# Performance work log

Hardware: AMD Instinct MI355X
Metric: run time of the kernel (lower is better)

## Reference

```python
import jax, jax.numpy as jnp
import numpy as np
from jax import lax

K = 8            # number of object slots
H = 250          # hidden / fc_size
EPS = 1e-5
DN = ('NCHW', 'OIHW', 'NCHW')


def ln_all(x):
    # F.layer_norm over all non-batch dims, no affine params (torch init: w=1,b=0)
    ax = tuple(range(1, x.ndim))
    m = jnp.mean(x, ax, keepdims=True)
    v = jnp.var(x, ax, keepdims=True)
    return (x - m) * lax.rsqrt(v + EPS)


def ln_last(x):
    # nn.LayerNorm(feat) -> last dim only
    m = jnp.mean(x, -1, keepdims=True)
    v = jnp.var(x, -1, keepdims=True)
    return (x - m) * lax.rsqrt(v + EPS)


def conv(x, w, b):
    # torch Conv2d(k=4, s=2, p=1), NCHW
    y = lax.conv_general_dilated(x, w, (2, 2), [(1, 1), (1, 1)], dimension_numbers=DN)
    return y + b[None, :, None, None]


def up4(x):
    return jnp.repeat(jnp.repeat(x, 4, axis=2), 4, axis=3)


def setup_inputs():
    ks = jax.random.split(jax.random.key(0), 20)
    bk = 48 * K
    p = lambda i, shape, s: jax.random.normal(ks[i], shape, jnp.float32) * s
    z = lambda n: jnp.zeros((n,), jnp.float32)
    return dict(
        x=p(0, (bk, 4096), 1.0),
        state=p(1, (bk, H), 1.0),
        # encoder convs (OIHW) + fc
        c1w=p(2, (16, 1, 4, 4), 0.25), c1b=z(16),
        c2w=p(3, (32, 16, 4, 4), 0.06), c2b=z(32),
        c3w=p(4, (64, 32, 4, 4), 0.04), c3b=z(64),
        efc_w=p(5, (4096, 512), 0.016), efc_b=z(512),
        # R_NEM (weights stored as [in, out])
        renc_w=p(6, (H, H), 0.06), renc_b=z(H),
        core_w=p(7, (2 * H, H), 0.045), core_b=z(H),
        ctx_w=p(8, (H, H), 0.06), ctx_b=z(H),
        att1_w=p(9, (H, 100), 0.06), att1_b=z(100),
        att2_w=p(10, (100, 1), 0.1), att2_b=z(1),
        out_w=p(11, (2 * H + 512, H), 0.03), out_b=z(H),
        # decoder fcs + convs
        dfc1_w=p(12, (H, 512), 0.06), dfc1_b=z(512),
        dfc2_w=p(13, (512, 4096), 0.045), dfc2_b=z(4096),
        d1w=p(14, (32, 64, 4, 4), 0.03), d1b=z(32),
        d2w=p(15, (16, 32, 4, 4), 0.045), d2b=z(16),
        d3w=p(16, (1, 16, 4, 4), 0.06), d3b=z(1),
    )


def reference(x, state, c1w, c1b, c2w, c2b, c3w, c3b, efc_w, efc_b,
              renc_w, renc_b, core_w, core_b, ctx_w, ctx_b,
              att1_w, att1_b, att2_w, att2_b, out_w, out_b,
              dfc1_w, dfc1_b, dfc2_w, dfc2_b, d1w, d1b, d2w, d2b, d3w, d3b):
    bk = x.shape[0]
    b = bk // K

    # ---------------- EncoderLayer ----------------
    def inwrap(h, w, bias):  # InputWrapper conv branch: NHWC -> permute(0,3,2,1) -> conv -> back
        y = conv(jnp.transpose(h, (0, 3, 2, 1)), w, bias)
        return jax.nn.elu(ln_all(jnp.transpose(y, (0, 3, 2, 1))))

    h = x.reshape(bk, 64, 64, 1)
    h = inwrap(h, c1w, c1b)                 # (bk,32,32,16)
    h = inwrap(h, c2w, c2b)                 # (bk,16,16,32)
    h = inwrap(h, c3w, c3b)                 # (bk,8,8,64)
    h = h.reshape(bk, -1)                   # (bk,4096)
    h = jax.nn.elu(ln_last(h @ efc_w + efc_b))   # (bk,512)

    # ---------------- R_NEM (RecurrentLayer) ----------------
    s1 = jax.nn.relu(ln_last(state @ renc_w + renc_b))   # (bk,H)
    s1r = s1.reshape(b, K, H)
    idx = np.array([[j for j in range(K) if j != i] for i in range(K)])  # (K,K-1)
    cs = s1r[:, idx, :]                                    # context: (b,K,K-1,H)
    fs = jnp.broadcast_to(s1r[:, :, None, :], cs.shape)    # focus copies
    pair = jnp.concatenate([fs, cs], axis=-1)              # (b,K,K-1,2H)
    core = jax.nn.relu(ln_last(pair @ core_w + core_b))    # (b,K,K-1,H)
    ctx = jax.nn.relu(ln_last(core @ ctx_w + ctx_b))       # (b,K,K-1,H)
    att = jax.nn.sigmoid(jnp.tanh(ln_last(core @ att1_w + att1_b)) @ att2_w + att2_b)  # (b,K,K-1,1)
    effect = jnp.sum(ctx * att, axis=2).reshape(bk, H)     # attention-weighted sum over K-1
    total = jnp.concatenate([s1, effect, h], axis=1)       # (bk, 2H+512)
    new_state = total @ out_w + out_b                      # (bk,H)
    xr = jax.nn.sigmoid(ln_last(new_state))
    state_out = jax.nn.sigmoid(new_state)

    # ---------------- DecoderLayer ----------------
    d = jax.nn.relu(ln_last(xr @ dfc1_w + dfc1_b))         # (bk,512)
    d = jax.nn.relu(ln_last(d @ dfc2_w + dfc2_b))          # (bk,4096)
    d = d.reshape(bk, 8, 8, 64)

    def outwrap(t, w, bias):
        y = conv(up4(jnp.transpose(t, (0, 3, 2, 1))), w, bias)
        return jnp.transpose(y, (0, 3, 2, 1))

    d = jax.nn.relu(ln_all(outwrap(d, d1w, d1b)))          # (bk,16,16,32)
    d = jax.nn.relu(ln_all(outwrap(d, d2w, d2b)))          # (bk,32,32,16)
    d = jax.nn.sigmoid(outwrap(d, d3w, d3b))               # (bk,64,64,1), no LN
    x_out = d.reshape(bk, -1)                              # (bk,4096)
    return x_out, state_out
```

## Files before the change

### kernel.cpp

```cpp
#include <hip/hip_runtime.h>
#include <hip/hip_bf16.h>
#include <math.h>

typedef __attribute__((ext_vector_type(8))) short bf16x8;
typedef __attribute__((ext_vector_type(4))) float f32x4;

__device__ __forceinline__ float eluf(float v){ return v > 0.f ? v : expm1f(v); }
__device__ __forceinline__ float sigf(float v){ return 1.f/(1.f+expf(-v)); }
__device__ __forceinline__ unsigned short f2bf(float f){
  unsigned u = __float_as_uint(f);
  u += 0x7FFFu + ((u >> 16) & 1u);
  return (unsigned short)(u >> 16);
}
__device__ __forceinline__ float bf2f(short s){
  return __uint_as_float(((unsigned)(unsigned short)s) << 16);
}

__device__ __forceinline__ void block_reduce2(float& a, float& b, float* sbuf){
  __syncthreads();
  for (int off = 32; off; off >>= 1){
    a += __shfl_down(a, off);
    b += __shfl_down(b, off);
  }
  int lane = threadIdx.x & 63, w = threadIdx.x >> 6;
  if (lane == 0){ sbuf[2*w] = a; sbuf[2*w+1] = b; }
  __syncthreads();
  if (threadIdx.x == 0){
    int nw = blockDim.x >> 6;
    float sa = 0.f, sb = 0.f;
    for (int i = 0; i < nw; i++){ sa += sbuf[2*i]; sb += sbuf[2*i+1]; }
    sbuf[0] = sa; sbuf[1] = sb;
  }
  __syncthreads();
  a = sbuf[0]; b = sbuf[1];
}

__device__ __forceinline__ float fold_sum(const float* __restrict__ w, int O, int I,
                                          int o, int i, int pa, int pb, int da, int db){
  float s = 0.f;
  for (int kh = 0; kh < 4; kh++){
    bool inh = (pb==0) ? (db==0 ? (kh==0) : (kh>=1)) : (db==0 ? (kh<=2) : (kh==3));
    if (!inh) continue;
    for (int kw = 0; kw < 4; kw++){
      bool inw = (pa==0) ? (da==0 ? (kw==0) : (kw>=1)) : (da==0 ? (kw<=2) : (kw==3));
      if (!inw) continue;
      s += w[((o*I + i)*4 + kh)*4 + kw];
    }
  }
  return s;
}
__device__ __forceinline__ void fold_elem(const float* __restrict__ w, float* __restrict__ CW,
                                          int O, int I, int l){
  int o = l % O; int q = l / O;
  int da = q & 1, db = (q>>1)&1, pa = (q>>2)&1, pb = (q>>3)&1, i = q>>4;
  CW[(((pb*2+pa)*4 + db*2+da)*I + i)*O + o] = fold_sum(w, O, I, o, i, pa, pb, da, db);
}
__device__ __forceinline__ void cvtc2_elem(const float* __restrict__ w, short* __restrict__ D, int l){
  int i = l & 15, t = (l>>4) & 15, o = l>>8;
  D[l] = (short)f2bf(w[(o*16 + i)*16 + t]);
}
__device__ __forceinline__ void cvtc3_elem(const float* __restrict__ w, short* __restrict__ D, int l){
  int i = l & 31, t = (l>>5) & 15, o = l>>9;
  D[l] = (short)f2bf(w[(o*32 + i)*16 + t]);
}
__device__ __forceinline__ void foldd1_elem(const float* __restrict__ w, short* __restrict__ D, int l){
  int i = l & 63, tap = (l>>6)&3, o = (l>>8)&31, ph = l>>13;
  D[l] = (short)f2bf(fold_sum(w, 32, 64, o, i, ph&1, ph>>1, tap&1, tap>>1));
}
__device__ __forceinline__ void foldd2_elem(const float* __restrict__ w, short* __restrict__ D, int l){
  int i = l & 31, tap = (l>>5)&3, o = (l>>7)&15, ph = l>>11;
  D[l] = (short)f2bf(fold_sum(w, 16, 32, o, i, ph&1, ph>>1, tap&1, tap>>1));
}

__global__ __launch_bounds__(256) void prep_combined(
  const float* __restrict__ efc,  short* __restrict__ Defc,
  const float* __restrict__ dfc2, short* __restrict__ Ddfc2,
  const float* __restrict__ outw, short* __restrict__ Dout,
  const float* __restrict__ corew,short* __restrict__ Dcore,
  const float* __restrict__ dfc1, short* __restrict__ Ddfc1,
  const float* __restrict__ renc, short* __restrict__ Drenc,
  const float* __restrict__ ctx,  short* __restrict__ Dctx,
  const float* __restrict__ att1, short* __restrict__ Datt1,
  const float* __restrict__ d3w, float* __restrict__ CWT3,
  const float* __restrict__ c2w, short* __restrict__ BtC2,
  const float* __restrict__ c3w, short* __restrict__ BtC3,
  const float* __restrict__ d1w, short* __restrict__ BD1,
  const float* __restrict__ d2w, short* __restrict__ BD2,
  const float* __restrict__ state, short* __restrict__ SBF,
  short* __restrict__ TOTb)
{
  int bx = blockIdx.x;
  if (bx >= 1192){
    const int F3=256, P2=F3+8192, P3=P2+32768, P4=P3+32768, P5=P4+8192,
              ST=P5+98304, TOTAL=ST+4608;
    for (int l = (bx-1192)*256 + threadIdx.x; l < TOTAL; l += 256*256){
      if (l < F3)      fold_elem(d3w, CWT3, 1, 16, l);
      else if (l < P2) cvtc2_elem(c2w, BtC2, l - F3);
      else if (l < P3) cvtc3_elem(c3w, BtC3, l - P2);
      else if (l < P4) foldd1_elem(d1w, BD1, l - P3);
      else if (l < P5) foldd2_elem(d2w, BD2, l - P4);
      else if (l < ST){
        int q = l - P5;
        int n = q >> 8, k = q & 255;
        SBF[q] = (k < 250) ? (short)f2bf(state[n*250 + k]) : (short)0;
      } else {
        int q = l - ST;
        int row = q / 12, cc = q % 12;
        int col = cc < 6 ? 250 + cc : 506 + (cc - 6);
        TOTb[row*1024 + col] = 0;
      }
    }
    return;
  }
  const float* W; short* D; int K, N, Kp, base, mode = 0;
  if      (bx < 512) { W=efc;  D=Defc;  K=4096; N=512;  Kp=4096; base=0;    }
  else if (bx < 1024){ W=dfc2; D=Ddfc2; K=512;  N=4096; Kp=512;  base=512;  }
  else if (bx < 1088){ W=outw; D=Dout;  K=1012; N=250;  Kp=1024; base=1024; mode=2; }
  else if (bx < 1120){ W=corew;D=Dcore; K=500;  N=250;  Kp=512;  base=1088; mode=1; }
  else if (bx < 1152){ W=dfc1; D=Ddfc1; K=250;  N=512;  Kp=256;  base=1120; }
  else if (bx < 1168){ W=renc; D=Drenc; K=250;  N=250;  Kp=256;  base=1152; }
  else if (bx < 1184){ W=ctx;  D=Dctx;  K=250;  N=250;  Kp=256;  base=1168; }
  else               { W=att1; D=Datt1; K=250;  N=100;  Kp=256;  base=1184; }
  int t = bx - base;
  int tpr = Kp >> 6;
  int tk = t % tpr, tn = t / tpr;
  __shared__ short tile[64][65];
  int c = threadIdx.x & 63, r4 = threadIdx.x >> 6;
  int n0 = tn*64, k0 = tk*64;
  #pragma unroll 4
  for (int p = 0; p < 16; p++){
    int r = r4*16 + p;
    int k = k0 + r, n = n0 + c;
    int ksrc = k; bool valid;
    if (mode == 0) valid = (k < K);
    else if (mode == 1){ valid = (k < 250) || (k >= 256 && k < 506); ksrc = k < 256 ? k : k - 6; }
    else { valid = (k < 250) || (k >= 256 && k < 506) || (k >= 512);
           ksrc = k < 256 ? k : (k < 512 ? k - 6 : k - 12); }
    float v = (valid && n < N) ? W[(size_t)ksrc*N + n] : 0.f;
    tile[c][r] = (short)f2bf(v);
  }
  __syncthreads();
  #pragma unroll 4
  for (int p = 0; p < 16; p++){
    int nn = r4*16 + p;
    int n = n0 + nn;
    if (n < N) D[(size_t)n*Kp + k0 + c] = tile[nn][c];
  }
}

__global__ __launch_bounds__(256) void gemm_mfma(
    const short* __restrict__ Ab, const short* __restrict__ Bt,
    float* __restrict__ P, int M, int N, int Kp, int Kc)
{
  __shared__ __align__(16) short As[64*32];
  __shared__ __align__(16) short Bs[64*32];
  int tid = threadIdx.x;
  int bm = blockIdx.y*64, bn = blockIdx.x*64;
  int kb = blockIdx.z * Kc;
  int kend = kb + Kc;

  int r = tid >> 2, c = tid & 3;
  const short* Arow = Ab + (size_t)(bm + r)*Kp;
  int gn = bn + r;
  bool bval = gn < N;
  const short* Brow = Bt + (size_t)gn*Kp;

  uint4 hA, hB;
  auto load_regs = [&](int k0){
    hA = *(const uint4*)&Arow[k0 + c*8];
    hB = bval ? *(const uint4*)&Brow[k0 + c*8] : make_uint4(0,0,0,0);
  };
  auto write_lds = [&](){
    *(uint4*)&As[r*32 + c*8] = hA;
    *(uint4*)&Bs[r*32 + c*8] = hB;
  };

  int wave = tid >> 6;
  int ln = tid & 15, quad = (tid >> 4) & 3;
  int wr = (wave >> 1) * 32, wc = (wave & 1) * 32;

  f32x4 zero = {0.f, 0.f, 0.f, 0.f};
  f32x4 acc[2][2] = {{zero, zero}, {zero, zero}};

  load_regs(kb);
  write_lds();
  __syncthreads();
  for (int k0 = kb; k0 < kend; k0 += 32){
    int nxt = k0 + 32;
    if (nxt < kend) load_regs(nxt);
    bf16x8 a0 = *(const bf16x8*)&As[(wr +      ln)*32 + quad*8];
    bf16x8 a1 = *(const bf16x8*)&As[(wr + 16 + ln)*32 + quad*8];
    bf16x8 b0 = *(const bf16x8*)&Bs[(wc +      ln)*32 + quad*8];
    bf16x8 b1 = *(const bf16x8*)&Bs[(wc + 16 + ln)*32 + quad*8];
    acc[0][0] = __builtin_amdgcn_mfma_f32_16x16x32_bf16(a0, b0, acc[0][0], 0, 0, 0);
    acc[0][1] = __builtin_amdgcn_mfma_f32_16x16x32_bf16(a0, b1, acc[0][1], 0, 0, 0);
    acc[1][0] = __builtin_amdgcn_mfma_f32_16x16x32_bf16(a1, b0, acc[1][0], 0, 0, 0);
    acc[1][1] = __builtin_amdgcn_mfma_f32_16x16x32_bf16(a1, b1, acc[1][1], 0, 0, 0);
    __syncthreads();
    if (nxt < kend){ write_lds(); __syncthreads(); }
  }

  float* Pout = P + (size_t)blockIdx.z*M*N;
  #pragma unroll
  for (int t = 0; t < 2; t++)
    #pragma unroll
    for (int u = 0; u < 2; u++)
      #pragma unroll
      for (int j = 0; j < 4; j++){
        int row = bm + wr + t*16 + quad*4 + j;
        int col = bn + wc + u*16 + ln;
        if (col < N) Pout[(size_t)row*N + col] = acc[t][u][j];
      }
}

__global__ __launch_bounds__(256) void gemm_core_mfma(
    const short* __restrict__ Tb, const short* __restrict__ Bt,
    float* __restrict__ P, int M, int N, int Kc)
{
  __shared__ __align__(16) short As[64*32];
  __shared__ __align__(16) short Bs[64*32];
  int tid = threadIdx.x;
  int bm = blockIdx.y*64, bn = blockIdx.x*64;
  int kb = blockIdx.z * Kc;
  int kend = kb + Kc;

  int r = tid >> 2, c = tid & 3;
  int gr = bm + r;
  int jj2 = gr % 7, fi2 = gr / 7;
  int ii = fi2 & 7, j2 = fi2 >> 3;
  int jidx = jj2 < ii ? jj2 : jj2 + 1;
  const short* own = Tb + (size_t)fi2*1024;
  const short* oth = Tb + (size_t)(j2*8 + jidx)*1024;
  int gn = bn + r;
  bool bval = gn < N;
  const short* Brow = Bt + (size_t)gn*512;

  uint4 hA, hB;
  auto load_regs = [&](int k0){
    int kk = k0 + c*8;
    const short* src = (kk & 256) ? oth : own;
    hA = *(const uint4*)&src[kk & 255];
    hB = bval ? *(const uint4*)&Brow[kk] : make_uint4(0,0,0,0);
  };
  auto write_lds = [&](){
    *(uint4*)&As[r*32 + c*8] = hA;
    *(uint4*)&Bs[r*32 + c*8] = hB;
  };

  int wave = tid >> 6;
  int ln = tid & 15, quad = (tid >> 4) & 3;
  int wr = (wave >> 1) * 32, wc = (wave & 1) * 32;

  f32x4 zero = {0.f, 0.f, 0.f, 0.f};
  f32x4 acc[2][2] = {{zero, zero}, {zero, zero}};

  load_regs(kb);
  write_lds();
  __syncthreads();
  for (int k0 = kb; k0 < kend; k0 += 32){
    int nxt = k0 + 32;
    if (nxt < kend) load_regs(nxt);
    bf16x8 a0 = *(const bf16x8*)&As[(wr +      ln)*32 + quad*8];
    bf16x8 a1 = *(const bf16x8*)&As[(wr + 16 + ln)*32 + quad*8];
    bf16x8 b0 = *(const bf16x8*)&Bs[(wc +      ln)*32 + quad*8];
    bf16x8 b1 = *(const bf16x8*)&Bs[(wc + 16 + ln)*32 + quad*8];
    acc[0][0] = __builtin_amdgcn_mfma_f32_16x16x32_bf16(a0, b0, acc[0][0], 0, 0, 0);
    acc[0][1] = __builtin_amdgcn_mfma_f32_16x16x32_bf16(a0, b1, acc[0][1], 0, 0, 0);
    acc[1][0] = __builtin_amdgcn_mfma_f32_16x16x32_bf16(a1, b0, acc[1][0], 0, 0, 0);
    acc[1][1] = __builtin_amdgcn_mfma_f32_16x16x32_bf16(a1, b1, acc[1][1], 0, 0, 0);
    __syncthreads();
    if (nxt < kend){ write_lds(); __syncthreads(); }
  }

  float* Pout = P + (size_t)blockIdx.z*M*N;
  #pragma unroll
  for (int t = 0; t < 2; t++)
    #pragma unroll
    for (int u = 0; u < 2; u++)
      #pragma unroll
      for (int j = 0; j < 4; j++){
        int row = bm + wr + t*16 + quad*4 + j;
        int col = bn + wc + u*16 + ln;
        if (col < N) Pout[(size_t)row*N + col] = acc[t][u][j];
      }
}

__global__ __launch_bounds__(256) void reduce_ln(
    const float* __restrict__ Pp, const float* __restrict__ bias,
    void* __restrict__ outp, int M, int N, int KS, int os, int act, int obf)
{
  __shared__ float rowbuf[4096];
  __shared__ float sbuf[16];
  int row = blockIdx.x;
  size_t MN = (size_t)M*N;
  float s = 0.f, s2 = 0.f;
  for (int c = threadIdx.x; c < N; c += 256){
    float v = bias[c];
    for (int ks = 0; ks < KS; ks++) v += Pp[ks*MN + (size_t)row*N + c];
    rowbuf[c] = v; s += v; s2 += v*v;
  }
  block_reduce2(s, s2, sbuf);
  float m = s / N;
  float r = rsqrtf(s2/N - m*m + 1e-5f);
  for (int c = threadIdx.x; c < N; c += 256){
    float v = (rowbuf[c]-m)*r;
    if (act == 1) v = fmaxf(v, 0.f);
    else if (act == 2) v = eluf(v);
    else if (act == 3) v = tanhf(v);
    if (obf) ((short*)outp)[(size_t)row*os + c] = f2bf(v);
    else     ((float*)outp)[(size_t)row*os + c] = v;
  }
}

__global__ __launch_bounds__(256) void reduce_ns(
    const float* __restrict__ Pp, const float* __restrict__ bias,
    short* __restrict__ XRb, float* __restrict__ so, int M, int N, int KS)
{
  __shared__ float rowbuf[256];
  __shared__ float sbuf[16];
  int row = blockIdx.x;
  size_t MN = (size_t)M*N;
  float s = 0.f, s2 = 0.f;
  for (int c = threadIdx.x; c < N; c += 256){
    float v = bias[c];
    for (int ks = 0; ks < KS; ks++) v += Pp[ks*MN + (size_t)row*N + c];
    rowbuf[c] = v; s += v; s2 += v*v;
  }
  block_reduce2(s, s2, sbuf);
  float m = s / N;
  float r = rsqrtf(s2/N - m*m + 1e-5f);
  for (int c = threadIdx.x; c < N; c += 256){
    float v = rowbuf[c];
    XRb[(size_t)row*256 + c] = f2bf(sigf((v-m)*r));
    so[(size_t)row*N + c] = sigf(v);
  }
}

__global__ __launch_bounds__(448) void ctx_att_effect(
    const float* __restrict__ Pc, const float* __restrict__ ctx_b,
    const float* __restrict__ Pa, const float* __restrict__ att1_b,
    const float* __restrict__ w2, const float* __restrict__ b2,
    short* __restrict__ tot)
{
  __shared__ float ctxs[7][250];
  __shared__ float att_s[7];
  int fi = blockIdx.x, tid = threadIdx.x;
  int jj = tid >> 6, lane = tid & 63;
  const size_t MN = (size_t)2688*250, MN2 = (size_t)2688*100;
  int row = fi*7 + jj;
  float vv[4];
  float s = 0.f, s2 = 0.f;
  #pragma unroll
  for (int t = 0; t < 4; t++){
    int c = lane + t*64;
    float v = 0.f;
    if (c < 250) v = ctx_b[c] + Pc[(size_t)row*250 + c] + Pc[MN + (size_t)row*250 + c];
    vv[t] = v; s += v; s2 += v*v;
  }
  #pragma unroll
  for (int off = 32; off; off >>= 1){ s += __shfl_down(s, off); s2 += __shfl_down(s2, off); }
  s = __shfl(s, 0); s2 = __shfl(s2, 0);
  float m = s*(1.f/250.f);
  float r = rsqrtf(s2*(1.f/250.f) - m*m + 1e-5f);
  #pragma unroll
  for (int t = 0; t < 4; t++){
    int c = lane + t*64;
    if (c < 250) ctxs[jj][c] = fmaxf((vv[t]-m)*r, 0.f);
  }
  float va[2];
  s = 0.f; s2 = 0.f;
  #pragma unroll
  for (int t = 0; t < 2; t++){
    int c = lane + t*64;
    float v = 0.f;
    if (c < 100){
      v = att1_b[c];
      #pragma unroll
      for (int ks = 0; ks < 4; ks++) v += Pa[ks*MN2 + (size_t)row*100 + c];
    }
    va[t] = v; s += v; s2 += v*v;
  }
  #pragma unroll
  for (int off = 32; off; off >>= 1){ s += __shfl_down(s, off); s2 += __shfl_down(s2, off); }
  s = __shfl(s, 0); s2 = __shfl(s2, 0);
  m = s*0.01f;
  r = rsqrtf(s2*0.01f - m*m + 1e-5f);
  float d = 0.f;
  #pragma unroll
  for (int t = 0; t < 2; t++){
    int c = lane + t*64;
    if (c < 100) d += tanhf((va[t]-m)*r)*w2[c];
  }
  #pragma unroll
  for (int off = 32; off; off >>= 1) d += __shfl_down(d, off);
  if (lane == 0) att_s[jj] = sigf(d + b2[0]);
  __syncthreads();
  for (int h = tid; h < 250; h += 448){
    float sum = 0.f;
    #pragma unroll
    for (int q = 0; q < 7; q++) sum += ctxs[q][h]*att_s[q];
    tot[(size_t)fi*1024 + 256 + h] = f2bf(sum);
  }
}

__global__ __launch_bounds__(256) void enc_conv1_ig(
    const float* __restrict__ x, const float* __restrict__ w, const float* __restrict__ bias,
    short* __restrict__ outp)
{
  __shared__ __align__(16) float in_t[66*68];
  __shared__ short rawb[16384];
  __shared__ float sbuf[16];
  int n = blockIdx.x, tid = threadIdx.x;
  for (int l = tid; l < 66*68; l += 256) in_t[l] = 0.f;
  __syncthreads();
  const float* xin = x + (size_t)n*4096;
  for (int l4 = tid; l4 < 1024; l4 += 256){
    float4 v = *(const float4*)&xin[l4*4];
    int aa = (l4*4) >> 6, bb = (l4*4) & 63;
    float* dst = &in_t[(aa+1)*68 + bb + 1];
    dst[0]=v.x; dst[1]=v.y; dst[2]=v.z; dst[3]=v.w;
  }
  int o = tid & 15;
  float wr[16];
  #pragma unroll
  for (int t = 0; t < 16; t++) wr[t] = w[o*16 + t];
  float bv = bias[o];
  __syncthreads();
  float s = 0.f, s2 = 0.f;
  for (int r = 0; r < 64; r++){
    int idx = tid + (r<<8);
    int bq = (idx>>4)&31, aq = idx>>9;
    int a0 = 2*aq, b0 = 2*bq;
    float acc = bv;
    #pragma unroll
    for (int kw = 0; kw < 4; kw++){
      const float* row = &in_t[(a0+kw)*68 + b0];
      float2 p0 = *(const float2*)&row[0];
      float2 p1 = *(const float2*)&row[2];
      acc += p0.x*wr[0*4+kw] + p0.y*wr[1*4+kw] + p1.x*wr[2*4+kw] + p1.y*wr[3*4+kw];
    }
    rawb[idx] = f2bf(acc);
    s += acc; s2 += acc*acc;
  }
  block_reduce2(s, s2, sbuf);
  float m = s*(1.f/16384.f);
  float rs = rsqrtf(s2*(1.f/16384.f) - m*m + 1e-5f);
  short* op = outp + (size_t)n*16384;
  for (int l = tid; l < 16384; l += 256){
    float v = bf2f(rawb[l]);
    op[l] = f2bf(eluf((v-m)*rs));
  }
}

__global__ __launch_bounds__(256) void enc_conv23_mfma(
    const short* __restrict__ in, const short* __restrict__ Bt2, const float* __restrict__ bias2,
    const short* __restrict__ Bt3, const float* __restrict__ bias3, short* __restrict__ outp)
{
  __shared__ __align__(16) short smem[34*34*16];
  __shared__ float sbuf[16];
  int n = blockIdx.x, tid = threadIdx.x;
  for (int l = tid; l < 34*34*16/4; l += 256) ((unsigned long long*)smem)[l] = 0ull;
  __syncthreads();
  const short* ip = in + (size_t)n*16384;
  for (int l = tid; l < 4096; l += 256){
    int i4 = l & 3, bb = (l>>2) & 31, aa = l>>7;
    *(uint2*)&smem[((aa+1)*34 + (bb+1))*16 + i4*4] = *(const uint2*)&ip[aa*512 + bb*16 + i4*4];
  }
  int wave = tid>>6, ln = tid&15, quad = (tid>>4)&3;
  bf16x8 bfr[2][8];
  #pragma unroll
  for (int nt = 0; nt < 2; nt++){
    const short* Brow = Bt2 + (nt*16 + ln)*256;
    #pragma unroll
    for (int ks = 0; ks < 8; ks++)
      bfr[nt][ks] = *(const bf16x8*)&Brow[ks*32 + quad*8];
  }
  __syncthreads();
  f32x4 z = {0.f,0.f,0.f,0.f};
  f32x4 acc[2][4] = {{z,z,z,z},{z,z,z,z}};
  int tapq = quad>>1, io = (quad&1)*8;
  #pragma unroll
  for (int ks = 0; ks < 8; ks++){
    int t = 2*ks + tapq;
    int kh = t>>2, kw = t&3;
    #pragma unroll
    for (int mt = 0; mt < 4; mt++){
      int p = (wave*4 + mt)*16 + ln;
      int oa = p>>4, ob = p&15;
      bf16x8 a = *(const bf16x8*)&smem[((2*oa+kw)*34 + (2*ob+kh))*16 + io];
      acc[0][mt] = __builtin_amdgcn_mfma_f32_16x16x32_bf16(a, bfr[0][ks], acc[0][mt],0,0,0);
      acc[1][mt] = __builtin_amdgcn_mfma_f32_16x16x32_bf16(a, bfr[1][ks], acc[1][mt],0,0,0);
    }
  }
  float s = 0.f, s2 = 0.f;
  #pragma unroll
  for (int nt = 0; nt < 2; nt++){
    float bz = bias2[nt*16 + ln];
    #pragma unroll
    for (int mt = 0; mt < 4; mt++)
      #pragma unroll
      for (int j = 0; j < 4; j++){
        float v = acc[nt][mt][j] + bz;
        acc[nt][mt][j] = v; s += v; s2 += v*v;
      }
  }
  block_reduce2(s, s2, sbuf);
  float m2 = s*(1.f/8192.f);
  float rs2 = rsqrtf(s2*(1.f/8192.f) - m2*m2 + 1e-5f);
  int o3 = wave*16 + ln;
  bf16x8 bfr3[16];
  {
    const short* Brow = Bt3 + o3*512;
    #pragma unroll
    for (int ks = 0; ks < 16; ks++)
      bfr3[ks] = *(const bf16x8*)&Brow[ks*32 + quad*8];
  }
  for (int l = tid; l < 2592; l += 256) ((unsigned long long*)smem)[l] = 0ull;
  __syncthreads();
  #pragma unroll
  for (int nt = 0; nt < 2; nt++){
    int o = nt*16 + ln;
    #pragma unroll
    for (int mt = 0; mt < 4; mt++)
      #pragma unroll
      for (int j = 0; j < 4; j++){
        int p = (wave*4 + mt)*16 + quad*4 + j;
        int oa = p>>4, ob = p&15;
        smem[((oa+1)*18 + (ob+1))*32 + o] = f2bf(eluf((acc[nt][mt][j]-m2)*rs2));
      }
  }
  __syncthreads();
  f32x4 acc3[4] = {z,z,z,z};
  #pragma unroll
  for (int ks = 0; ks < 16; ks++){
    int kh = ks>>2, kw = ks&3;
    #pragma unroll
    for (int mt = 0; mt < 4; mt++){
      int p = mt*16 + ln;
      int oa = p>>3, ob = p&7;
      bf16x8 a = *(const bf16x8*)&smem[((2*oa+kw)*18 + (2*ob+kh))*32 + quad*8];
      acc3[mt] = __builtin_amdgcn_mfma_f32_16x16x32_bf16(a, bfr3[ks], acc3[mt],0,0,0);
    }
  }
  s = 0.f; s2 = 0.f;
  float bz3 = bias3[o3];
  #pragma unroll
  for (int mt = 0; mt < 4; mt++)
    #pragma unroll
    for (int j = 0; j < 4; j++){
      float v = acc3[mt][j] + bz3;
      acc3[mt][j] = v; s += v; s2 += v*v;
    }
  block_reduce2(s, s2, sbuf);
  float m3 = s*(1.f/4096.f);
  float rs3 = rsqrtf(s2*(1.f/4096.f) - m3*m3 + 1e-5f);
  short* op = outp + (size_t)n*4096;
  #pragma unroll
  for (int mt = 0; mt < 4; mt++)
    #pragma unroll
    for (int j = 0; j < 4; j++){
      int p = mt*16 + quad*4 + j;
      int oa = p>>3, ob = p&7;
      op[oa*512 + ob*64 + o3] = f2bf(eluf((acc3[mt][j]-m3)*rs3));
    }
}

__global__ __launch_bounds__(256) void dec_conv12_mfma(
    const short* __restrict__ in, const short* __restrict__ Bd1, const float* __restrict__ bias1,
    const short* __restrict__ Bd2, const float* __restrict__ bias2, short* __restrict__ outp)
{
  __shared__ __align__(16) short smem[18*18*32];
  __shared__ float sbuf[16];
  int n = blockIdx.x, tid = threadIdx.x;
  for (int l = tid; l < 1600; l += 256) ((unsigned long long*)smem)[l] = 0ull;
  __syncthreads();
  const short* ip = in + (size_t)n*4096;
  for (int l = tid; l < 1024; l += 256){
    int i4 = l & 15, sb = (l>>4)&7, sa = l>>7;
    *(uint2*)&smem[((sa+1)*10 + (sb+1))*64 + i4*4] = *(const uint2*)&ip[sa*512 + sb*64 + i4*4];
  }
  int wave = tid>>6, ln = tid&15, quad = (tid>>4)&3;
  int pa = wave & 1, pb = wave >> 1;
  bf16x8 bfr1[2][8];
  #pragma unroll
  for (int nt = 0; nt < 2; nt++){
    const short* Brow = Bd1 + (wave*32 + nt*16 + ln)*256;
    #pragma unroll
    for (int ks = 0; ks < 8; ks++)
      bfr1[nt][ks] = *(const bf16x8*)&Brow[ks*32 + quad*8];
  }
  __syncthreads();
  f32x4 z = {0.f,0.f,0.f,0.f};
  f32x4 acc[2][4] = {{z,z,z,z},{z,z,z,z}};
  #pragma unroll
  for (int ks = 0; ks < 8; ks++){
    int tap = ks>>1, ibase = (ks&1)*32 + quad*8;
    int da = tap & 1, db = tap >> 1;
    #pragma unroll
    for (int mt = 0; mt < 4; mt++){
      int p = mt*16 + ln;
      int ta = p>>3, tb = p&7;
      bf16x8 a = *(const bf16x8*)&smem[((ta+da+pa)*10 + (tb+db+pb))*64 + ibase];
      acc[0][mt] = __builtin_amdgcn_mfma_f32_16x16x32_bf16(a, bfr1[0][ks], acc[0][mt],0,0,0);
      acc[1][mt] = __builtin_amdgcn_mfma_f32_16x16x32_bf16(a, bfr1[1][ks], acc[1][mt],0,0,0);
    }
  }
  float s = 0.f, s2 = 0.f;
  #pragma unroll
  for (int nt = 0; nt < 2; nt++){
    float bz = bias1[nt*16 + ln];
    #pragma unroll
    for (int mt = 0; mt < 4; mt++)
      #pragma unroll
      for (int j = 0; j < 4; j++){
        float v = acc[nt][mt][j] + bz;
        acc[nt][mt][j] = v; s += v; s2 += v*v;
      }
  }
  block_reduce2(s, s2, sbuf);
  float m1 = s*(1.f/8192.f);
  float rs1 = rsqrtf(s2*(1.f/8192.f) - m1*m1 + 1e-5f);
  bf16x8 bfr2[4];
  {
    const short* Brow = Bd2 + (wave*16 + ln)*128;
    #pragma unroll
    for (int ks = 0; ks < 4; ks++)
      bfr2[ks] = *(const bf16x8*)&Brow[ks*32 + quad*8];
  }
  for (int l = tid; l < 2592; l += 256) ((unsigned long long*)smem)[l] = 0ull;
  __syncthreads();
  #pragma unroll
  for (int nt = 0; nt < 2; nt++){
    int o = nt*16 + ln;
    #pragma unroll
    for (int mt = 0; mt < 4; mt++)
      #pragma unroll
      for (int j = 0; j < 4; j++){
        int p = mt*16 + quad*4 + j;
        int ta = p>>3, tb = p&7;
        int sa = 2*ta + pa, sb = 2*tb + pb;
        smem[((sa+1)*18 + (sb+1))*32 + o] = f2bf(fmaxf((acc[nt][mt][j]-m1)*rs1, 0.f));
      }
  }
  __syncthreads();
  f32x4 acc2[16] = {z,z,z,z,z,z,z,z,z,z,z,z,z,z,z,z};
  #pragma unroll
  for (int ks = 0; ks < 4; ks++){
    int da = ks & 1, db = ks >> 1;
    #pragma unroll
    for (int mt = 0; mt < 16; mt++){
      int p = mt*16 + ln;
      int ta = p>>4, tb = p&15;
      bf16x8 a = *(const bf16x8*)&smem[((ta+da+pa)*18 + (tb+db+pb))*32 + quad*8];
      acc2[mt] = __builtin_amdgcn_mfma_f32_16x16x32_bf16(a, bfr2[ks], acc2[mt],0,0,0);
    }
  }
  s = 0.f; s2 = 0.f;
  float bz2 = bias2[ln];
  #pragma unroll
  for (int mt = 0; mt < 16; mt++)
    #pragma unroll
    for (int j = 0; j < 4; j++){
      float v = acc2[mt][j] + bz2;
      acc2[mt][j] = v; s += v; s2 += v*v;
    }
  block_reduce2(s, s2, sbuf);
  float m = s*(1.f/16384.f);
  float rs = rsqrtf(s2*(1.f/16384.f) - m*m + 1e-5f);
  short* op = outp + (size_t)n*16384;
  #pragma unroll
  for (int mt = 0; mt < 16; mt++)
    #pragma unroll
    for (int j = 0; j < 4; j++){
      int p = mt*16 + quad*4 + j;
      int ta = p>>4, tb = p&15;
      op[(2*ta+pa)*512 + (2*tb+pb)*16 + ln] = f2bf(fmaxf((acc2[mt][j]-m)*rs, 0.f));
    }
}

__global__ __launch_bounds__(256) void dec_conv3_ig(
    const short* __restrict__ in, const float* __restrict__ CWT, const float* __restrict__ bias,
    float* __restrict__ outp)
{
  __shared__ __align__(16) float in_t[9792];
  __shared__ __align__(16) float wl[256];
  int bx = blockIdx.x;
  int n = bx >> 1, b0 = (bx & 1) * 32, tb0 = b0 >> 1;
  int tid = threadIdx.x;
  const short* ip = in + (size_t)n*16384;
  for (int l = tid; l < 9792; l += 256){
    int i = l & 15, sb = (l >> 4) % 18, sap = l / 288;
    int sa = sap - 1, sbg = tb0 - 1 + sb;
    float v = 0.f;
    if ((unsigned)sa < 32u && (unsigned)sbg < 32u)
      v = bf2f(ip[sa*512 + sbg*16 + i]);
    in_t[(sap*18 + sb)*16 + i] = v;
  }
  for (int l = tid; l < 256; l += 256) wl[l] = CWT[l];
  __syncthreads();
  float bv = bias[0];
  int bl = tid & 31, ath = tid >> 5;
  int b = b0 + bl;
  int tb = b >> 1, pb = b & 1;
  float* op = outp + (size_t)n*4096;
  #pragma unroll
  for (int j = 0; j < 8; j++){
    int a = ath*8 + j;
    int ta = a >> 1, pa = a & 1;
    float4 s4 = make_float4(0.f,0.f,0.f,0.f);
    #pragma unroll
    for (int db = 0; db < 2; db++){
      int sb = tb + db + (pb ? 0 : -1);
      int sbl = sb - (tb0 - 1);
      #pragma unroll
      for (int da = 0; da < 2; da++){
        int sa = ta + da + (pa ? 0 : -1);
        int sap = sa + 1;
        const float4* A4 = (const float4*)&in_t[(sap*18 + sbl)*16];
        const float4* B4 = (const float4*)&wl[((pb*2+pa)*4 + db*2+da)*16];
        #pragma unroll
        for (int q = 0; q < 4; q++){
          float4 av = A4[q], bw = B4[q];
          s4.x += av.x*bw.x; s4.y += av.y*bw.y;
          s4.z += av.z*bw.z; s4.w += av.w*bw.w;
        }
      }
    }
    op[a*64 + b] = sigf(bv + s4.x + s4.y + s4.z + s4.w);
  }
}

extern "C" void kernel_launch(void* const* d_in, const int* in_sizes, int n_in,
                              void* d_out, int out_size, void* d_ws, size_t ws_size,
                              hipStream_t stream) {
  const float* x      = (const float*)d_in[0];
  const float* state  = (const float*)d_in[1];
  const float* c1w    = (const float*)d_in[2];
  const float* c1b    = (const float*)d_in[3];
  const float* c2w    = (const float*)d_in[4];
  const float* c2b    = (const float*)d_in[5];
  const float* c3w    = (const float*)d_in[6];
  const float* c3b    = (const float*)d_in[7];
  const float* efc_w  = (const float*)d_in[8];
  const float* efc_b  = (const float*)d_in[9];
  const float* renc_w = (const float*)d_in[10];
  const float* renc_b = (const float*)d_in[11];
  const float* core_w = (const float*)d_in[12];
  const float* core_b = (const float*)d_in[13];
  const float* ctx_w  = (const float*)d_in[14];
  const float* ctx_b  = (const float*)d_in[15];
  const float* att1_w = (const float*)d_in[16];
  const float* att1_b = (const float*)d_in[17];
  const float* att2_w = (const float*)d_in[18];
  const float* att2_b = (const float*)d_in[19];
  const float* out_w  = (const float*)d_in[20];
  const float* out_b  = (const float*)d_in[21];
  const float* dfc1_w = (const float*)d_in[22];
  const float* dfc1_b = (const float*)d_in[23];
  const float* dfc2_w = (const float*)d_in[24];
  const float* dfc2_b = (const float*)d_in[25];
  const float* d1w    = (const float*)d_in[26];
  const float* d1b    = (const float*)d_in[27];
  const float* d2w    = (const float*)d_in[28];
  const float* d2b    = (const float*)d_in[29];
  const float* d3w    = (const float*)d_in[30];
  const float* d3b    = (const float*)d_in[31];

  float* wsf = (float*)d_ws;
  size_t o = 0;
  float* PB   = wsf + o; o += (size_t)1600*1024;
  float* PB2  = wsf + o; o += (size_t)2688*100*4;
  float* CWT3 = wsf + o; o += 256;
  short* E1b  = (short*)(wsf + o); o += (size_t)384*16384/2;
  short* E2b  = (short*)(wsf + o); o += (size_t)384*8192/2;
  short* E3b  = (short*)(wsf + o); o += (size_t)384*4096/2;
  short* TOTb = (short*)(wsf + o); o += (size_t)384*1024/2;
  short* C1b  = (short*)(wsf + o); o += (size_t)2688*256/2;
  short* XRb  = (short*)(wsf + o); o += (size_t)384*256/2;
  short* G1b  = (short*)(wsf + o); o += (size_t)384*512/2;
  short* SBF  = (short*)(wsf + o); o += (size_t)384*256/2;
  short* BtC2 = (short*)(wsf + o); o += 8192/2;
  short* BtC3 = (short*)(wsf + o); o += 32768/2;
  short* BD1  = (short*)(wsf + o); o += 32768/2;
  short* BD2  = (short*)(wsf + o); o += 8192/2;
  short* BT_efc  = (short*)(wsf + o); o += 2097152/2;
  short* BT_renc = (short*)(wsf + o); o += 64000/2;
  short* BT_core = (short*)(wsf + o); o += 128000/2;
  short* BT_ctx  = (short*)(wsf + o); o += 64000/2;
  short* BT_att1 = (short*)(wsf + o); o += 25600/2;
  short* BT_out  = (short*)(wsf + o); o += 256000/2;
  short* BT_dfc1 = (short*)(wsf + o); o += 131072/2;
  short* BT_dfc2 = (short*)(wsf + o); o += 2097152/2;
  short* D2b = E1b;
  short* G2b = E3b;
  (void)E2b;

  float* xout = (float*)d_out;
  float* sout = xout + (size_t)384*4096;

  prep_combined<<<1448, 256, 0, stream>>>(
      efc_w, BT_efc, dfc2_w, BT_dfc2, out_w, BT_out, core_w, BT_core,
      dfc1_w, BT_dfc1, renc_w, BT_renc, ctx_w, BT_ctx, att1_w, BT_att1,
      d3w, CWT3, c2w, BtC2, c3w, BtC3, d1w, BD1, d2w, BD2, state, SBF, TOTb);

  enc_conv1_ig<<<384, 256, 0, stream>>>(x, c1w, c1b, E1b);
  enc_conv23_mfma<<<384, 256, 0, stream>>>(E1b, BtC2, c2b, BtC3, c3b, E3b);
  gemm_mfma<<<dim3(8,6,8), 256, 0, stream>>>(E3b, BT_efc, PB, 384, 512, 4096, 512);
  reduce_ln<<<384, 256, 0, stream>>>(PB, efc_b, TOTb+512, 384, 512, 8, 1024, 2, 1);

  gemm_mfma<<<dim3(4,6,8), 256, 0, stream>>>(SBF, BT_renc, PB, 384, 250, 256, 32);
  reduce_ln<<<384, 256, 0, stream>>>(PB, renc_b, TOTb, 384, 250, 8, 1024, 1, 1);
  gemm_core_mfma<<<dim3(4,42,2), 256, 0, stream>>>(TOTb, BT_core, PB, 2688, 250, 256);
  reduce_ln<<<2688, 256, 0, stream>>>(PB, core_b, C1b, 2688, 250, 2, 256, 1, 1);
  gemm_mfma<<<dim3(4,42,2), 256, 0, stream>>>(C1b, BT_ctx, PB, 2688, 250, 256, 128);
  gemm_mfma<<<dim3(2,42,4), 256, 0, stream>>>(C1b, BT_att1, PB2, 2688, 100, 256, 64);
  ctx_att_effect<<<384, 448, 0, stream>>>(PB, ctx_b, PB2, att1_b, att2_w, att2_b, TOTb);

  gemm_mfma<<<dim3(4,6,8), 256, 0, stream>>>(TOTb, BT_out, PB, 384, 250, 1024, 128);
  reduce_ns<<<384, 256, 0, stream>>>(PB, out_b, XRb, sout, 384, 250, 8);

  gemm_mfma<<<dim3(8,6,4), 256, 0, stream>>>(XRb, BT_dfc1, PB, 384, 512, 256, 64);
  reduce_ln<<<384, 256, 0, stream>>>(PB, dfc1_b, G1b, 384, 512, 4, 512, 1, 1);
  gemm_mfma<<<dim3(64,6,1), 256, 0, stream>>>(G1b, BT_dfc2, PB, 384, 4096, 512, 512);
  reduce_ln<<<384, 256, 0, stream>>>(PB, dfc2_b, G2b, 384, 4096, 1, 4096, 1, 1);

  dec_conv12_mfma<<<384, 256, 0, stream>>>(G2b, BD1, d1b, BD2, d2b, D2b);
  dec_conv3_ig<<<768, 256, 0, stream>>>(D2b, CWT3, d3b, xout);

  (void)in_sizes; (void)n_in; (void)out_size; (void)ws_size;
}
```

Baseline: 324.1 us.

## Split fused encoder conv2/conv3 kernel into implicit-GEMM kernels plus LN passes

Replaces the single per-sample fused conv2+LN+ELU+conv3+LN+ELU kernel with separate implicit-GEMM MFMA kernels for conv2 and conv3, a standalone LN/ELU pass for conv2, and the existing reduce_ln for conv3 (with a bias mask for channel-periodic bias). The intent is more parallelism and better MFMA tiling than the per-sample fused kernel, which held weights in registers and was limited to one block per sample. In exchange it adds intermediate global round-trips (bf16 conv2 output, fp32 conv3 partials) and extra launches.

```diff
diff --git a/kernel.cpp b/kernel.cpp
--- a/kernel.cpp
+++ b/kernel.cpp
@@ -213,6 +213,168 @@
       }
 }
 
+__global__ __launch_bounds__(256) void gemm_conv2g(
+    const short* __restrict__ In, const short* __restrict__ Bt,
+    short* __restrict__ Out)
+{
+  __shared__ __align__(16) short As[128*32];
+  __shared__ __align__(16) short Bs[32*32];
+  int tid = threadIdx.x;
+  int bm = blockIdx.x*128;
+
+  int ra = tid >> 1, ca = (tid & 1)*16;
+  int gr = bm + ra;
+  int n = gr >> 8, pos = gr & 255;
+  int oa = pos >> 4, ob = pos & 15;
+  const short* ibase = In + (size_t)n*16384;
+  int rb = tid >> 2, cb = (tid & 3)*8;
+  const short* Brow = Bt + rb*256;
+  bool bact = tid < 128;
+
+  uint4 hA0, hA1, hB;
+  auto load_regs = [&](int k0){
+    #pragma unroll
+    for (int h = 0; h < 2; h++){
+      int k = k0 + ca + h*8;
+      int tap = k >> 4;
+      int ai = 2*oa + (tap & 3) - 1, bi = 2*ob + (tap >> 2) - 1;
+      bool v = ((unsigned)ai < 32u) && ((unsigned)bi < 32u);
+      uint4 tv = v ? *(const uint4*)&ibase[ai*512 + bi*16 + (k & 15)] : make_uint4(0,0,0,0);
+      if (h == 0) hA0 = tv; else hA1 = tv;
+    }
+    if (bact) hB = *(const uint4*)&Brow[k0 + cb];
+  };
+  auto write_lds = [&](){
+    *(uint4*)&As[ra*32 + ca] = hA0;
+    *(uint4*)&As[ra*32 + ca + 8] = hA1;
+    if (bact) *(uint4*)&Bs[rb*32 + cb] = hB;
+  };
+
+  int wave = tid >> 6, ln = tid & 15, quad = (tid >> 4) & 3;
+  int wr = wave * 32;
+
+  f32x4 zero = {0.f,0.f,0.f,0.f};
+  f32x4 acc[2][2] = {{zero,zero},{zero,zero}};
+  load_regs(0); write_lds(); __syncthreads();
+  for (int k0 = 0; k0 < 256; k0 += 32){
+    int nxt = k0 + 32;
+    if (nxt < 256) load_regs(nxt);
+    bf16x8 a0 = *(const bf16x8*)&As[(wr +      ln)*32 + quad*8];
+    bf16x8 a1 = *(const bf16x8*)&As[(wr + 16 + ln)*32 + quad*8];
+    bf16x8 b0 = *(const bf16x8*)&Bs[(     ln)*32 + quad*8];
+    bf16x8 b1 = *(const bf16x8*)&Bs[(16 + ln)*32 + quad*8];
+    acc[0][0] = __builtin_amdgcn_mfma_f32_16x16x32_bf16(a0, b0, acc[0][0], 0, 0, 0);
+    acc[0][1] = __builtin_amdgcn_mfma_f32_16x16x32_bf16(a0, b1, acc[0][1], 0, 0, 0);
+    acc[1][0] = __builtin_amdgcn_mfma_f32_16x16x32_bf16(a1, b0, acc[1][0], 0, 0, 0);
+    acc[1][1] = __builtin_amdgcn_mfma_f32_16x16x32_bf16(a1, b1, acc[1][1], 0, 0, 0);
+    __syncthreads();
+    if (nxt < 256){ write_lds(); __syncthreads(); }
+  }
+  #pragma unroll
+  for (int t = 0; t < 2; t++)
+    #pragma unroll
+    for (int u = 0; u < 2; u++)
+      #pragma unroll
+      for (int j = 0; j < 4; j++){
+        int row = bm + wr + t*16 + quad*4 + j;
+        int col = u*16 + ln;
+        Out[(size_t)row*32 + col] = (short)f2bf(acc[t][u][j]);
+      }
+}
+
+__global__ __launch_bounds__(256) void ln_conv2_act(
+    short* __restrict__ E, const float* __restrict__ bias)
+{
+  __shared__ float sbuf[16];
+  int n = blockIdx.x, tid = threadIdx.x;
+  short* p = E + (size_t)n*8192;
+  float vv[32];
+  float s = 0.f, s2 = 0.f;
+  #pragma unroll
+  for (int t = 0; t < 4; t++){
+    bf16x8 v8 = *(const bf16x8*)&p[(t*256 + tid)*8];
+    #pragma unroll
+    for (int j = 0; j < 8; j++){
+      int i = (t*256 + tid)*8 + j;
+      float v = bf2f(v8[j]) + bias[i & 31];
+      vv[t*8+j] = v; s += v; s2 += v*v;
+    }
+  }
+  block_reduce2(s, s2, sbuf);
+  float m = s*(1.f/8192.f);
+  float rs = rsqrtf(s2*(1.f/8192.f) - m*m + 1e-5f);
+  #pragma unroll
+  for (int t = 0; t < 4; t++){
+    bf16x8 o8;
+    #pragma unroll
+    for (int j = 0; j < 8; j++)
+      o8[j] = (short)f2bf(eluf((vv[t*8+j]-m)*rs));
+    *(bf16x8*)&p[(t*256 + tid)*8] = o8;
+  }
+}
+
+__global__ __launch_bounds__(256) void gemm_conv3g(
+    const short* __restrict__ In, const short* __restrict__ Bt,
+    float* __restrict__ P)
+{
+  __shared__ __align__(16) short As[64*32];
+  __shared__ __align__(16) short Bs[64*32];
+  int tid = threadIdx.x;
+  int bm = blockIdx.x*64;
+
+  int r = tid >> 2, c = tid & 3;
+  int gr = bm + r;
+  int n = gr >> 6, pos = gr & 63;
+  int oa = pos >> 3, ob = pos & 7;
+  const short* ibase = In + (size_t)n*8192;
+  const short* Brow = Bt + r*512;
+
+  uint4 hA, hB;
+  auto load_regs = [&](int k0){
+    int k = k0 + c*8;
+    int tap = k >> 5;
+    int ai = 2*oa + (tap & 3) - 1, bi = 2*ob + (tap >> 2) - 1;
+    bool v = ((unsigned)ai < 16u) && ((unsigned)bi < 16u);
+    hA = v ? *(const uint4*)&ibase[(ai*16 + bi)*32 + (k & 31)] : make_uint4(0,0,0,0);
+    hB = *(const uint4*)&Brow[k];
+  };
+  auto write_lds = [&](){
+    *(uint4*)&As[r*32 + c*8] = hA;
+    *(uint4*)&Bs[r*32 + c*8] = hB;
+  };
+
+  int wave = tid >> 6, ln = tid & 15, quad = (tid >> 4) & 3;
+  int wr = (wave >> 1) * 32, wc = (wave & 1) * 32;
+
+  f32x4 zero = {0.f,0.f,0.f,0.f};
+  f32x4 acc[2][2] = {{zero,zero},{zero,zero}};
+  load_regs(0); write_lds(); __syncthreads();
+  for (int k0 = 0; k0 < 512; k0 += 32){
+    int nxt = k0 + 32;
+    if (nxt < 512) load_regs(nxt);
+    bf16x8 a0 = *(const bf16x8*)&As[(wr +      ln)*32 + quad*8];
+    bf16x8 a1 = *(const bf16x8*)&As[(wr + 16 + ln)*32 + quad*8];
+    bf16x8 b0 = *(const bf16x8*)&Bs[(wc +      ln)*32 + quad*8];
+    bf16x8 b1 = *(const bf16x8*)&Bs[(wc + 16 + ln)*32 + quad*8];
+    acc[0][0] = __builtin_amdgcn_mfma_f32_16x16x32_bf16(a0, b0, acc[0][0], 0, 0, 0);
+    acc[0][1] = __builtin_amdgcn_mfma_f32_16x16x32_bf16(a0, b1, acc[0][1], 0, 0, 0);
+    acc[1][0] = __builtin_amdgcn_mfma_f32_16x16x32_bf16(a1, b0, acc[1][0], 0, 0, 0);
+    acc[1][1] = __builtin_amdgcn_mfma_f32_16x16x32_bf16(a1, b1, acc[1][1], 0, 0, 0);
+    __syncthreads();
+    if (nxt < 512){ write_lds(); __syncthreads(); }
+  }
+  #pragma unroll
+  for (int t = 0; t < 2; t++)
+    #pragma unroll
+    for (int u = 0; u < 2; u++)
+      #pragma unroll
+      for (int j = 0; j < 4; j++){
+        int row = bm + wr + t*16 + quad*4 + j;
+        int col = wc + u*16 + ln;
+        P[(size_t)row*64 + col] = acc[t][u][j];
+      }
+}
+
 __global__ __launch_bounds__(256) void gemm_core_mfma(
     const short* __restrict__ Tb, const short* __restrict__ Bt,
     float* __restrict__ P, int M, int N, int Kc)
@@ -287,7 +449,7 @@
 
 __global__ __launch_bounds__(256) void reduce_ln(
     const float* __restrict__ Pp, const float* __restrict__ bias,
-    void* __restrict__ outp, int M, int N, int KS, int os, int act, int obf)
+    void* __restrict__ outp, int M, int N, int KS, int os, int act, int obf, int bmask)
 {
   __shared__ float rowbuf[4096];
   __shared__ float sbuf[16];
@@ -295,7 +457,7 @@
   size_t MN = (size_t)M*N;
   float s = 0.f, s2 = 0.f;
   for (int c = threadIdx.x; c < N; c += 256){
-    float v = bias[c];
+    float v = bias[c & bmask];
     for (int ks = 0; ks < KS; ks++) v += Pp[ks*MN + (size_t)row*N + c];
     rowbuf[c] = v; s += v; s2 += v*v;
   }
@@ -450,119 +612,6 @@
     float v = bf2f(rawb[l]);
     op[l] = f2bf(eluf((v-m)*rs));
   }
-}
-
-__global__ __launch_bounds__(256) void enc_conv23_mfma(
-    const short* __restrict__ in, const short* __restrict__ Bt2, const float* __restrict__ bias2,
-    const short* __restrict__ Bt3, const float* __restrict__ bias3, short* __restrict__ outp)
-{
-  __shared__ __align__(16) short smem[34*34*16];
-  __shared__ float sbuf[16];
-  int n = blockIdx.x, tid = threadIdx.x;
-  for (int l = tid; l < 34*34*16/4; l += 256) ((unsigned long long*)smem)[l] = 0ull;
-  __syncthreads();
-  const short* ip = in + (size_t)n*16384;
-  for (int l = tid; l < 4096; l += 256){
-    int i4 = l & 3, bb = (l>>2) & 31, aa = l>>7;
-    *(uint2*)&smem[((aa+1)*34 + (bb+1))*16 + i4*4] = *(const uint2*)&ip[aa*512 + bb*16 + i4*4];
-  }
-  int wave = tid>>6, ln = tid&15, quad = (tid>>4)&3;
-  bf16x8 bfr[2][8];
-  #pragma unroll
-  for (int nt = 0; nt < 2; nt++){
-    const short* Brow = Bt2 + (nt*16 + ln)*256;
-    #pragma unroll
-    for (int ks = 0; ks < 8; ks++)
-      bfr[nt][ks] = *(const bf16x8*)&Brow[ks*32 + quad*8];
-  }
-  __syncthreads();
-  f32x4 z = {0.f,0.f,0.f,0.f};
-  f32x4 acc[2][4] = {{z,z,z,z},{z,z,z,z}};
-  int tapq = quad>>1, io = (quad&1)*8;
-  #pragma unroll
-  for (int ks = 0; ks < 8; ks++){
-    int t = 2*ks + tapq;
-    int kh = t>>2, kw = t&3;
-    #pragma unroll
-    for (int mt = 0; mt < 4; mt++){
-      int p = (wave*4 + mt)*16 + ln;
-      int oa = p>>4, ob = p&15;
-      bf16x8 a = *(const bf16x8*)&smem[((2*oa+kw)*34 + (2*ob+kh))*16 + io];
-      acc[0][mt] = __builtin_amdgcn_mfma_f32_16x16x32_bf16(a, bfr[0][ks], acc[0][mt],0,0,0);
-      acc[1][mt] = __builtin_amdgcn_mfma_f32_16x16x32_bf16(a, bfr[1][ks], acc[1][mt],0,0,0);
-    }
-  }
-  float s = 0.f, s2 = 0.f;
-  #pragma unroll
-  for (int nt = 0; nt < 2; nt++){
-    float bz = bias2[nt*16 + ln];
-    #pragma unroll
-    for (int mt = 0; mt < 4; mt++)
-      #pragma unroll
-      for (int j = 0; j < 4; j++){
-        float v = acc[nt][mt][j] + bz;
-        acc[nt][mt][j] = v; s += v; s2 += v*v;
-      }
-  }
-  block_reduce2(s, s2, sbuf);
-  float m2 = s*(1.f/8192.f);
-  float rs2 = rsqrtf(s2*(1.f/8192.f) - m2*m2 + 1e-5f);
-  int o3 = wave*16 + ln;
-  bf16x8 bfr3[16];
-  {
-    const short* Brow = Bt3 + o3*512;
-    #pragma unroll
-    for (int ks = 0; ks < 16; ks++)
-      bfr3[ks] = *(const bf16x8*)&Brow[ks*32 + quad*8];
-  }
-  for (int l = tid; l < 2592; l += 256) ((unsigned long long*)smem)[l] = 0ull;
-  __syncthreads();
-  #pragma unroll
-  for (int nt = 0; nt < 2; nt++){
-    int o = nt*16 + ln;
-    #pragma unroll
-    for (int mt = 0; mt < 4; mt++)
-      #pragma unroll
-      for (int j = 0; j < 4; j++){
-        int p = (wave*4 + mt)*16 + quad*4 + j;
-        int oa = p>>4, ob = p&15;
-        smem[((oa+1)*18 + (ob+1))*32 + o] = f2bf(eluf((acc[nt][mt][j]-m2)*rs2));
-      }
-  }
-  __syncthreads();
-  f32x4 acc3[4] = {z,z,z,z};
-  #pragma unroll
-  for (int ks = 0; ks < 16; ks++){
-    int kh = ks>>2, kw = ks&3;
-    #pragma unroll
-    for (int mt = 0; mt < 4; mt++){
-      int p = mt*16 + ln;
-      int oa = p>>3, ob = p&7;
-      bf16x8 a = *(const bf16x8*)&smem[((2*oa+kw)*18 + (2*ob+kh))*32 + quad*8];
-      acc3[mt] = __builtin_amdgcn_mfma_f32_16x16x32_bf16(a, bfr3[ks], acc3[mt],0,0,0);
-    }
-  }
-  s = 0.f; s2 = 0.f;
-  float bz3 = bias3[o3];
-  #pragma unroll
-  for (int mt = 0; mt < 4; mt++)
-    #pragma unroll
-    for (int j = 0; j < 4; j++){
-      float v = acc3[mt][j] + bz3;
-      acc3[mt][j] = v; s += v; s2 += v*v;
-    }
-  block_reduce2(s, s2, sbuf);
-  float m3 = s*(1.f/4096.f);
-  float rs3 = rsqrtf(s2*(1.f/4096.f) - m3*m3 + 1e-5f);
-  short* op = outp + (size_t)n*4096;
-  #pragma unroll
-  for (int mt = 0; mt < 4; mt++)
-    #pragma unroll
-    for (int j = 0; j < 4; j++){
-      int p = mt*16 + quad*4 + j;
-      int oa = p>>3, ob = p&7;
-      op[oa*512 + ob*64 + o3] = f2bf(eluf((acc3[mt][j]-m3)*rs3));
-    }
 }
 
 __global__ __launch_bounds__(256) void dec_conv12_mfma(
@@ -793,7 +842,6 @@
   short* BT_dfc2 = (short*)(wsf + o); o += 2097152/2;
   short* D2b = E1b;
   short* G2b = E3b;
-  (void)E2b;
 
   float* xout = (float*)d_out;
   float* sout = xout + (size_t)384*4096;
@@ -804,14 +852,17 @@
       d3w, CWT3, c2w, BtC2, c3w, BtC3, d1w, BD1, d2w, BD2, state, SBF, TOTb);
 
   enc_conv1_ig<<<384, 256, 0, stream>>>(x, c1w, c1b, E1b);
-  enc_conv23_mfma<<<384, 256, 0, stream>>>(E1b, BtC2, c2b, BtC3, c3b, E3b);
+  gemm_conv2g<<<768, 256, 0, stream>>>(E1b, BtC2, E2b);
+  ln_conv2_act<<<384, 256, 0, stream>>>(E2b, c2b);
+  gemm_conv3g<<<384, 256, 0, stream>>>(E2b, BtC3, PB);
+  reduce_ln<<<384, 256, 0, stream>>>(PB, c3b, E3b, 384, 4096, 1, 4096, 2, 1, 63);
   gemm_mfma<<<dim3(8,6,8), 256, 0, stream>>>(E3b, BT_efc, PB, 384, 512, 4096, 512);
-  reduce_ln<<<384, 256, 0, stream>>>(PB, efc_b, TOTb+512, 384, 512, 8, 1024, 2, 1);
+  reduce_ln<<<384, 256, 0, stream>>>(PB, efc_b, TOTb+512, 384, 512, 8, 1024, 2, 1, -1);
 
   gemm_mfma<<<dim3(4,6,8), 256, 0, stream>>>(SBF, BT_renc, PB, 384, 250, 256, 32);
-  reduce_ln<<<384, 256, 0, stream>>>(PB, renc_b, TOTb, 384, 250, 8, 1024, 1, 1);
+  reduce_ln<<<384, 256, 0, stream>>>(PB, renc_b, TOTb, 384, 250, 8, 1024, 1, 1, -1);
   gemm_core_mfma<<<dim3(4,42,2), 256, 0, stream>>>(TOTb, BT_core, PB, 2688, 250, 256);
-  reduce_ln<<<2688, 256, 0, stream>>>(PB, core_b, C1b, 2688, 250, 2, 256, 1, 1);
+  reduce_ln<<<2688, 256, 0, stream>>>(PB, core_b, C1b, 2688, 250, 2, 256, 1, 1, -1);
   gemm_mfma<<<dim3(4,42,2), 256, 0, stream>>>(C1b, BT_ctx, PB, 2688, 250, 256, 128);
   gemm_mfma<<<dim3(2,42,4), 256, 0, stream>>>(C1b, BT_att1, PB2, 2688, 100, 256, 64);
   ctx_att_effect<<<384, 448, 0, stream>>>(PB, ctx_b, PB2, att1_b, att2_w, att2_b, TOTb);
@@ -820,9 +871,9 @@
   reduce_ns<<<384, 256, 0, stream>>>(PB, out_b, XRb, sout, 384, 250, 8);
 
   gemm_mfma<<<dim3(8,6,4), 256, 0, stream>>>(XRb, BT_dfc1, PB, 384, 512, 256, 64);
-  reduce_ln<<<384, 256, 0, stream>>>(PB, dfc1_b, G1b, 384, 512, 4, 512, 1, 1);
+  reduce_ln<<<384, 256, 0, stream>>>(PB, dfc1_b, G1b, 384, 512, 4, 512, 1, 1, -1);
   gemm_mfma<<<dim3(64,6,1), 256, 0, stream>>>(G1b, BT_dfc2, PB, 384, 4096, 512, 512);
-  reduce_ln<<<384, 256, 0, stream>>>(PB, dfc2_b, G2b, 384, 4096, 1, 4096, 1, 1);
+  reduce_ln<<<384, 256, 0, stream>>>(PB, dfc2_b, G2b, 384, 4096, 1, 4096, 1, 1, -1);
 
   dec_conv12_mfma<<<384, 256, 0, stream>>>(G2b, BD1, d1b, BD2, d2b, D2b);
   dec_conv3_ig<<<768, 256, 0, stream>>>(D2b, CWT3, d3b, xout);
```

Measured after the change: 339.7 us. 4.8% more time.
